# Performance work log

Measured on AMD Instinct MI355X. Metric: run time of the kernel, lower is better.

## Reference

```python
import jax, jax.numpy as jnp
import numpy as np

WS = 8        # window size
NUM_HEADS = 4 # attention heads


def setup_inputs() -> dict:
    key = jax.random.key(0)
    k1, k2, k3 = jax.random.split(key, 3)
    B, N, C = 32, 4096, 128
    x = jax.random.normal(k1, (B, N, C), dtype=jnp.float32)
    w_qkv = jax.random.normal(k2, (3 * C, C), dtype=jnp.float32) * (C ** -0.5)
    w_proj = jax.random.normal(k3, (C, C), dtype=jnp.float32) * (C ** -0.5)
    b_proj = jnp.zeros((C,), dtype=jnp.float32)
    return {"x": x, "w_qkv": w_qkv, "w_proj": w_proj, "b_proj": b_proj, "H": 64, "W": 64}


def reference(x, w_qkv, w_proj, b_proj, H, W):
    B, N, C = x.shape
    ws, nh = WS, NUM_HEADS
    hd = C // nh
    scale = hd ** -0.5
    hg, wg = H // ws, W // ws
    G = hg * wg          # total windows
    S = ws * ws          # tokens per window
    # partition into windows: [B, hg, ws, wg, ws, C] -> [B, G, S, C]
    xg = x.reshape(B, hg, ws, wg, ws, C).transpose(0, 1, 3, 2, 4, 5).reshape(B, G, S, C)
    # qkv projection (no bias)
    qkv = jnp.einsum('bgsc,oc->bgso', xg, w_qkv)
    qkv = qkv.reshape(B, G, S, 3, nh, hd).transpose(3, 0, 1, 4, 2, 5)  # [3,B,G,nh,S,hd]
    q, k, v = qkv[0], qkv[1], qkv[2]
    attn = jnp.einsum('bgnsd,bgntd->bgnst', q, k) * scale
    attn = jax.nn.softmax(attn, axis=-1)
    out = jnp.einsum('bgnst,bgntd->bgnsd', attn, v)
    # [B,G,nh,S,hd] -> [B,G,S,C] -> un-window -> [B,N,C]
    out = out.transpose(0, 1, 3, 2, 4).reshape(B, hg, wg, ws, ws, C)
    out = out.transpose(0, 1, 3, 2, 4, 5).reshape(B, N, C)
    return jnp.einsum('bnc,oc->bno', out, w_proj) + b_proj
```

## Files before the change

### kernel.cpp

```cpp
#include <hip/hip_runtime.h>
#include <cstdint>

typedef short short8 __attribute__((ext_vector_type(8)));
typedef float floatx4 __attribute__((ext_vector_type(4)));
typedef unsigned short ushortx4 __attribute__((ext_vector_type(4)));

__device__ __forceinline__ unsigned short f2bf(float f) {
  union { float f; unsigned u; } v; v.f = f;
  unsigned r = v.u + 0x7FFFu + ((v.u >> 16) & 1u);
  return (unsigned short)(r >> 16);
}
__device__ __forceinline__ float bf2f(unsigned short h) {
  union { unsigned u; float f; } v; v.u = ((unsigned)h) << 16; return v.f;
}

#define MFMA16B(A, B, C) __builtin_amdgcn_mfma_f32_16x16x32_bf16((A), (B), (C), 0, 0, 0)

__global__ void __launch_bounds__(256) prep_weights(const float* __restrict__ wq,
                                                    const float* __restrict__ wp,
                                                    unsigned short* __restrict__ wq_h,
                                                    unsigned short* __restrict__ wp_h) {
  int i = blockIdx.x * 256 + threadIdx.x;
  if (i < 384 * 128) wq_h[i] = f2bf(wq[i]);
  if (i < 128 * 128) wp_h[i] = f2bf(wp[i]);
}

__global__ void __launch_bounds__(256, 2) win_attn(const float* __restrict__ x,
                                                   const unsigned short* __restrict__ wqh,
                                                   const unsigned short* __restrict__ wph,
                                                   const float* __restrict__ bias,
                                                   float* __restrict__ out) {
  __shared__ unsigned short Xh[64][136];
  __shared__ unsigned short Xl[64][136];
  __shared__ unsigned short Qs[64][40];
  __shared__ unsigned short Ks[64][40];
  __shared__ unsigned short Vt[32][72];
  __shared__ unsigned short Ps[64][72];
  __shared__ unsigned short Os[64][136];

  const int tid = threadIdx.x;
  const int bid = blockIdx.x;
  const int b = bid >> 6;
  const int g = bid & 63;
  const int gh = g >> 3, gw = g & 7;
  const size_t base = (size_t)b * 4096 * 128;

  {
    const int r = tid >> 2;
    const int c0 = (tid & 3) * 32;
    const int n = gh * 512 + (r >> 3) * 64 + gw * 8 + (r & 7);
    const float4* xp = (const float4*)(x + base + (size_t)n * 128 + c0);
#pragma unroll
    for (int i = 0; i < 8; ++i) {
      float4 v = xp[i];
      ushortx4 hv, lv;
      hv[0] = f2bf(v.x); lv[0] = f2bf(v.x - bf2f(hv[0]));
      hv[1] = f2bf(v.y); lv[1] = f2bf(v.y - bf2f(hv[1]));
      hv[2] = f2bf(v.z); lv[2] = f2bf(v.z - bf2f(hv[2]));
      hv[3] = f2bf(v.w); lv[3] = f2bf(v.w - bf2f(hv[3]));
      *(ushortx4*)&Xh[r][c0 + i * 4] = hv;
      *(ushortx4*)&Xl[r][c0 + i * 4] = lv;
    }
  }
  __syncthreads();

  const int wv = tid >> 6;
  const int lane = tid & 63;
  const int lr = lane & 15;
  const int lg = lane >> 4;

  short8 ah[4], al[4];
#pragma unroll
  for (int ks = 0; ks < 4; ++ks) {
    ah[ks] = *(const short8*)&Xh[16 * wv + lr][ks * 32 + lg * 8];
    al[ks] = *(const short8*)&Xl[16 * wv + lr][ks * 32 + lg * 8];
  }

  const float scale = 0.17677669529663687f;

#pragma unroll 1
  for (int h = 0; h < 4; ++h) {
#pragma unroll
    for (int m = 0; m < 3; ++m) {
#pragma unroll
      for (int j = 0; j < 2; ++j) {
        floatx4 acc = {0.f, 0.f, 0.f, 0.f};
        const unsigned short* wb =
            wqh + (size_t)(m * 128 + h * 32 + j * 16 + lr) * 128 + lg * 8;
#pragma unroll
        for (int ks = 0; ks < 4; ++ks) {
          short8 bw = *(const short8*)(wb + ks * 32);
          acc = MFMA16B(ah[ks], bw, acc);
          acc = MFMA16B(al[ks], bw, acc);
        }
#pragma unroll
        for (int r = 0; r < 4; ++r) {
          const int s = 16 * wv + 4 * lg + r;
          const int d = j * 16 + lr;
          const unsigned short hv = f2bf(acc[r]);
          if (m == 0)      Qs[s][d] = hv;
          else if (m == 1) Ks[s][d] = hv;
          else             Vt[d][s] = hv;
        }
      }
    }
    __syncthreads();

    floatx4 sc[4];
    {
      short8 bq = *(const short8*)&Qs[16 * wv + lr][lg * 8];
#pragma unroll
      for (int tt = 0; tt < 4; ++tt) {
        short8 ak = *(const short8*)&Ks[16 * tt + lr][lg * 8];
        floatx4 z = {0.f, 0.f, 0.f, 0.f};
        sc[tt] = MFMA16B(ak, bq, z);
      }
    }
    float mx = -1e30f;
#pragma unroll
    for (int tt = 0; tt < 4; ++tt)
#pragma unroll
      for (int r = 0; r < 4; ++r) mx = fmaxf(mx, sc[tt][r]);
    mx = fmaxf(mx, __shfl_xor(mx, 16));
    mx = fmaxf(mx, __shfl_xor(mx, 32));
    float p[4][4];
    float sum = 0.f;
#pragma unroll
    for (int tt = 0; tt < 4; ++tt)
#pragma unroll
      for (int r = 0; r < 4; ++r) {
        float e = __expf(scale * (sc[tt][r] - mx));
        p[tt][r] = e;
        sum += e;
      }
    sum += __shfl_xor(sum, 16);
    sum += __shfl_xor(sum, 32);
    const float inv = 1.f / sum;
#pragma unroll
    for (int tt = 0; tt < 4; ++tt) {
      ushortx4 pv;
#pragma unroll
      for (int r = 0; r < 4; ++r) pv[r] = f2bf(p[tt][r] * inv);
      *(ushortx4*)&Ps[16 * wv + lr][16 * tt + 4 * lg] = pv;
    }
    __syncthreads();

    floatx4 o0 = {0.f, 0.f, 0.f, 0.f}, o1 = {0.f, 0.f, 0.f, 0.f};
#pragma unroll
    for (int ks = 0; ks < 2; ++ks) {
      short8 bp  = *(const short8*)&Ps[16 * wv + lr][ks * 32 + lg * 8];
      short8 av0 = *(const short8*)&Vt[lr][ks * 32 + lg * 8];
      short8 av1 = *(const short8*)&Vt[16 + lr][ks * 32 + lg * 8];
      o0 = MFMA16B(av0, bp, o0);
      o1 = MFMA16B(av1, bp, o1);
    }
#pragma unroll
    for (int r = 0; r < 4; ++r) {
      const int s = 16 * wv + lr;
      Os[s][h * 32 + 4 * lg + r]      = f2bf(o0[r]);
      Os[s][h * 32 + 16 + 4 * lg + r] = f2bf(o1[r]);
    }
    __syncthreads();
  }

  short8 ao[4];
#pragma unroll
  for (int ks = 0; ks < 4; ++ks)
    ao[ks] = *(const short8*)&Os[16 * wv + lr][ks * 32 + lg * 8];
#pragma unroll
  for (int nt = 0; nt < 8; ++nt) {
    floatx4 acc = {0.f, 0.f, 0.f, 0.f};
    const unsigned short* wb = wph + (size_t)(nt * 16 + lr) * 128 + lg * 8;
#pragma unroll
    for (int ks = 0; ks < 4; ++ks)
      acc = MFMA16B(ao[ks], *(const short8*)(wb + ks * 32), acc);
    const float bb = bias[nt * 16 + lr];
#pragma unroll
    for (int r = 0; r < 4; ++r) {
      const int s = 16 * wv + 4 * lg + r;
      const int n = gh * 512 + (s >> 3) * 64 + gw * 8 + (s & 7);
      out[base + (size_t)n * 128 + nt * 16 + lr] = acc[r] + bb;
    }
  }
}

extern "C" void kernel_launch(void* const* d_in, const int* in_sizes, int n_in,
                              void* d_out, int out_size, void* d_ws, size_t ws_size,
                              hipStream_t stream) {
  (void)in_sizes; (void)n_in; (void)out_size; (void)ws_size;
  const float* x  = (const float*)d_in[0];
  const float* wq = (const float*)d_in[1];
  const float* wp = (const float*)d_in[2];
  const float* bp = (const float*)d_in[3];
  float* out = (float*)d_out;
  unsigned short* wq_h = (unsigned short*)d_ws;
  unsigned short* wp_h = wq_h + 384 * 128;
  prep_weights<<<192, 256, 0, stream>>>(wq, wp, wq_h, wp_h);
  win_attn<<<2048, 256, 0, stream>>>(x, wq_h, wp_h, bp, out);
}
```

Measured before the change: 242.1 us.

## Assign one attention head per wavefront and drop per-head block barriers

Work is now split by head instead of by token row. Each wavefront loads and splits the whole 64-token window of x from global memory into hi/lo bf16 fragments itself, computes Q/K/V for its own head, and runs softmax and P·V in private swizzled LDS regions with only compiler fences. This removes the four block-wide barriers per head and the shared X staging buffer, and it pre-scales Q. LDS is packed into one 48KB buffer and launch bounds are raised to 3 blocks per CU. In exchange, every wave reads all of x for the window (4x the global load traffic per block) and the per-wave fragment arrays raise register pressure.

```diff
diff --git a/kernel.cpp b/kernel.cpp
--- a/kernel.cpp
+++ b/kernel.cpp
@@ -15,6 +15,7 @@
 }
 
 #define MFMA16B(A, B, C) __builtin_amdgcn_mfma_f32_16x16x32_bf16((A), (B), (C), 0, 0, 0)
+#define LDS_FENCE() asm volatile("" ::: "memory")
 
 __global__ void __launch_bounds__(256) prep_weights(const float* __restrict__ wq,
                                                     const float* __restrict__ wp,
@@ -25,148 +26,187 @@
   if (i < 128 * 128) wp_h[i] = f2bf(wp[i]);
 }
 
-__global__ void __launch_bounds__(256, 2) win_attn(const float* __restrict__ x,
+__global__ void __launch_bounds__(256, 3) win_attn(const float* __restrict__ x,
                                                    const unsigned short* __restrict__ wqh,
                                                    const unsigned short* __restrict__ wph,
                                                    const float* __restrict__ bias,
                                                    float* __restrict__ out) {
-  __shared__ unsigned short Xh[64][136];
-  __shared__ unsigned short Xl[64][136];
-  __shared__ unsigned short Qs[64][40];
-  __shared__ unsigned short Ks[64][40];
-  __shared__ unsigned short Vt[32][72];
-  __shared__ unsigned short Ps[64][72];
-  __shared__ unsigned short Os[64][136];
+  __shared__ char smem[49152];
 
   const int tid = threadIdx.x;
+  const int wv = tid >> 6;
+  const int lane = tid & 63;
+  const int lr = lane & 15;
+  const int lg = lane >> 4;
+  const int swz = (lr & 7) << 4;
+
   const int bid = blockIdx.x;
   const int b = bid >> 6;
   const int g = bid & 63;
   const int gh = g >> 3, gw = g & 7;
-  const size_t base = (size_t)b * 4096 * 128;
-
-  {
-    const int r = tid >> 2;
-    const int c0 = (tid & 3) * 32;
-    const int n = gh * 512 + (r >> 3) * 64 + gw * 8 + (r & 7);
-    const float4* xp = (const float4*)(x + base + (size_t)n * 128 + c0);
-#pragma unroll
-    for (int i = 0; i < 8; ++i) {
-      float4 v = xp[i];
-      ushortx4 hv, lv;
-      hv[0] = f2bf(v.x); lv[0] = f2bf(v.x - bf2f(hv[0]));
-      hv[1] = f2bf(v.y); lv[1] = f2bf(v.y - bf2f(hv[1]));
-      hv[2] = f2bf(v.z); lv[2] = f2bf(v.z - bf2f(hv[2]));
-      hv[3] = f2bf(v.w); lv[3] = f2bf(v.w - bf2f(hv[3]));
-      *(ushortx4*)&Xh[r][c0 + i * 4] = hv;
-      *(ushortx4*)&Xl[r][c0 + i * 4] = lv;
-    }
-  }
-  __syncthreads();
-
-  const int wv = tid >> 6;
-  const int lane = tid & 63;
-  const int lr = lane & 15;
-  const int lg = lane >> 4;
-
-  short8 ah[4], al[4];
-#pragma unroll
-  for (int ks = 0; ks < 4; ++ks) {
-    ah[ks] = *(const short8*)&Xh[16 * wv + lr][ks * 32 + lg * 8];
-    al[ks] = *(const short8*)&Xl[16 * wv + lr][ks * 32 + lg * 8];
-  }
-
-  const float scale = 0.17677669529663687f;
-
-#pragma unroll 1
-  for (int h = 0; h < 4; ++h) {
+  const size_t base = (size_t)b * (4096 * 128);
+
+  char* regA = smem + wv * 8192;
+  char* regV = smem + 32768 + wv * 4096;
+  char* osb  = smem;
+
+  const float SCALE = 0.17677669529663687f;
+
+#pragma unroll
+  for (int mt = 0; mt < 4; ++mt) {
+    const int s = mt * 16 + lr;
+    const int n = gh * 512 + (s >> 3) * 64 + gw * 8 + (s & 7);
+    const float* xp = x + base + (size_t)n * 128 + lg * 8;
+    short8 ah[4], al[4];
+#pragma unroll
+    for (int ks = 0; ks < 4; ++ks) {
+      float4 u = *(const float4*)(xp + ks * 32);
+      float4 w = *(const float4*)(xp + ks * 32 + 4);
+      float f[8] = {u.x, u.y, u.z, u.w, w.x, w.y, w.z, w.w};
+      short8 hh, ll;
+#pragma unroll
+      for (int j = 0; j < 8; ++j) {
+        unsigned short hb = f2bf(f[j]);
+        hh[j] = (short)hb;
+        ll[j] = (short)f2bf(f[j] - bf2f(hb));
+      }
+      ah[ks] = hh;
+      al[ks] = ll;
+    }
 #pragma unroll
     for (int m = 0; m < 3; ++m) {
 #pragma unroll
-      for (int j = 0; j < 2; ++j) {
+      for (int jt = 0; jt < 2; ++jt) {
         floatx4 acc = {0.f, 0.f, 0.f, 0.f};
         const unsigned short* wb =
-            wqh + (size_t)(m * 128 + h * 32 + j * 16 + lr) * 128 + lg * 8;
+            wqh + (size_t)(m * 128 + wv * 32 + jt * 16 + lr) * 128 + lg * 8;
 #pragma unroll
         for (int ks = 0; ks < 4; ++ks) {
           short8 bw = *(const short8*)(wb + ks * 32);
           acc = MFMA16B(ah[ks], bw, acc);
           acc = MFMA16B(al[ks], bw, acc);
         }
-#pragma unroll
-        for (int r = 0; r < 4; ++r) {
-          const int s = 16 * wv + 4 * lg + r;
-          const int d = j * 16 + lr;
-          const unsigned short hv = f2bf(acc[r]);
-          if (m == 0)      Qs[s][d] = hv;
-          else if (m == 1) Ks[s][d] = hv;
-          else             Vt[d][s] = hv;
+        if (m == 2) {
+          ushortx4 vv;
+#pragma unroll
+          for (int r = 0; r < 4; ++r) vv[r] = f2bf(acc[r]);
+          const int d = jt * 16 + lr;
+          *(ushortx4*)(regV + ((d * 128 + mt * 32 + lg * 8) ^ swz)) = vv;
+        } else {
+#pragma unroll
+          for (int r = 0; r < 4; ++r) {
+            const int s0 = mt * 16 + 4 * lg + r;
+            const int col = (m ? 32 : 0) + jt * 16 + lr;
+            const float v = (m == 0) ? acc[r] * SCALE : acc[r];
+            *(unsigned short*)(regA + ((s0 * 128 + col * 2) ^ ((s0 & 7) << 4))) =
+                f2bf(v);
+          }
         }
       }
     }
-    __syncthreads();
-
-    floatx4 sc[4];
-    {
-      short8 bq = *(const short8*)&Qs[16 * wv + lr][lg * 8];
-#pragma unroll
-      for (int tt = 0; tt < 4; ++tt) {
-        short8 ak = *(const short8*)&Ks[16 * tt + lr][lg * 8];
-        floatx4 z = {0.f, 0.f, 0.f, 0.f};
-        sc[tt] = MFMA16B(ak, bq, z);
+  }
+
+  LDS_FENCE();
+
+  short8 kf[4], qf[4];
+#pragma unroll
+  for (int i = 0; i < 4; ++i) {
+    const int row = i * 16 + lr;
+    qf[i] = *(const short8*)(regA + ((row * 128 + 16 * lg) ^ swz));
+    kf[i] = *(const short8*)(regA + ((row * 128 + 64 + 16 * lg) ^ swz));
+  }
+  floatx4 sc[4][4];
+#pragma unroll
+  for (int mt = 0; mt < 4; ++mt)
+#pragma unroll
+    for (int nt = 0; nt < 4; ++nt) {
+      floatx4 z = {0.f, 0.f, 0.f, 0.f};
+      sc[mt][nt] = MFMA16B(kf[mt], qf[nt], z);
+    }
+
+  float mx[4], inv[4];
+#pragma unroll
+  for (int nt = 0; nt < 4; ++nt) {
+    float m0 = -1e30f;
+#pragma unroll
+    for (int mt = 0; mt < 4; ++mt)
+#pragma unroll
+      for (int r = 0; r < 4; ++r) m0 = fmaxf(m0, sc[mt][nt][r]);
+    m0 = fmaxf(m0, __shfl_xor(m0, 16));
+    m0 = fmaxf(m0, __shfl_xor(m0, 32));
+    mx[nt] = m0;
+  }
+#pragma unroll
+  for (int nt = 0; nt < 4; ++nt) {
+    float s0 = 0.f;
+#pragma unroll
+    for (int mt = 0; mt < 4; ++mt)
+#pragma unroll
+      for (int r = 0; r < 4; ++r) {
+        float e = __expf(sc[mt][nt][r] - mx[nt]);
+        sc[mt][nt][r] = e;
+        s0 += e;
       }
-    }
-    float mx = -1e30f;
-#pragma unroll
-    for (int tt = 0; tt < 4; ++tt)
-#pragma unroll
-      for (int r = 0; r < 4; ++r) mx = fmaxf(mx, sc[tt][r]);
-    mx = fmaxf(mx, __shfl_xor(mx, 16));
-    mx = fmaxf(mx, __shfl_xor(mx, 32));
-    float p[4][4];
-    float sum = 0.f;
-#pragma unroll
-    for (int tt = 0; tt < 4; ++tt)
-#pragma unroll
-      for (int r = 0; r < 4; ++r) {
-        float e = __expf(scale * (sc[tt][r] - mx));
-        p[tt][r] = e;
-        sum += e;
-      }
-    sum += __shfl_xor(sum, 16);
-    sum += __shfl_xor(sum, 32);
-    const float inv = 1.f / sum;
-#pragma unroll
-    for (int tt = 0; tt < 4; ++tt) {
+    s0 += __shfl_xor(s0, 16);
+    s0 += __shfl_xor(s0, 32);
+    inv[nt] = 1.f / s0;
+  }
+
+#pragma unroll
+  for (int nt = 0; nt < 4; ++nt) {
+    const int row = nt * 16 + lr;
+#pragma unroll
+    for (int mt = 0; mt < 4; ++mt) {
       ushortx4 pv;
 #pragma unroll
-      for (int r = 0; r < 4; ++r) pv[r] = f2bf(p[tt][r] * inv);
-      *(ushortx4*)&Ps[16 * wv + lr][16 * tt + 4 * lg] = pv;
-    }
-    __syncthreads();
-
-    floatx4 o0 = {0.f, 0.f, 0.f, 0.f}, o1 = {0.f, 0.f, 0.f, 0.f};
-#pragma unroll
-    for (int ks = 0; ks < 2; ++ks) {
-      short8 bp  = *(const short8*)&Ps[16 * wv + lr][ks * 32 + lg * 8];
-      short8 av0 = *(const short8*)&Vt[lr][ks * 32 + lg * 8];
-      short8 av1 = *(const short8*)&Vt[16 + lr][ks * 32 + lg * 8];
-      o0 = MFMA16B(av0, bp, o0);
-      o1 = MFMA16B(av1, bp, o1);
-    }
-#pragma unroll
-    for (int r = 0; r < 4; ++r) {
-      const int s = 16 * wv + lr;
-      Os[s][h * 32 + 4 * lg + r]      = f2bf(o0[r]);
-      Os[s][h * 32 + 16 + 4 * lg + r] = f2bf(o1[r]);
-    }
-    __syncthreads();
-  }
+      for (int r = 0; r < 4; ++r) pv[r] = f2bf(sc[mt][nt][r] * inv[nt]);
+      *(ushortx4*)(regA + ((row * 128 + mt * 32 + lg * 8) ^ swz)) = pv;
+    }
+  }
+
+  LDS_FENCE();
+
+  short8 vf[2][2], pf[4][2];
+#pragma unroll
+  for (int dt = 0; dt < 2; ++dt)
+#pragma unroll
+    for (int ks = 0; ks < 2; ++ks)
+      vf[dt][ks] = *(const short8*)(regV + (((16 * dt + lr) * 128 + ks * 64 + 16 * lg) ^ swz));
+#pragma unroll
+  for (int st = 0; st < 4; ++st)
+#pragma unroll
+    for (int ks = 0; ks < 2; ++ks)
+      pf[st][ks] = *(const short8*)(regA + (((16 * st + lr) * 128 + ks * 64 + 16 * lg) ^ swz));
+  floatx4 ot[2][4];
+#pragma unroll
+  for (int dt = 0; dt < 2; ++dt)
+#pragma unroll
+    for (int st = 0; st < 4; ++st) {
+      floatx4 z = {0.f, 0.f, 0.f, 0.f};
+      ot[dt][st] = z;
+#pragma unroll
+      for (int ks = 0; ks < 2; ++ks)
+        ot[dt][st] = MFMA16B(vf[dt][ks], pf[st][ks], ot[dt][st]);
+    }
+
+  __syncthreads();
+
+#pragma unroll
+  for (int st = 0; st < 4; ++st)
+#pragma unroll
+    for (int dt = 0; dt < 2; ++dt) {
+      ushortx4 ov;
+#pragma unroll
+      for (int r = 0; r < 4; ++r) ov[r] = f2bf(ot[dt][st][r]);
+      *(ushortx4*)(osb + (16 * st + lr) * 272 + (wv * 32 + dt * 16 + 4 * lg) * 2) = ov;
+    }
+
+  __syncthreads();
 
   short8 ao[4];
 #pragma unroll
   for (int ks = 0; ks < 4; ++ks)
-    ao[ks] = *(const short8*)&Os[16 * wv + lr][ks * 32 + lg * 8];
+    ao[ks] = *(const short8*)(osb + (16 * wv + lr) * 272 + ks * 64 + 16 * lg);
 #pragma unroll
   for (int nt = 0; nt < 8; ++nt) {
     floatx4 acc = {0.f, 0.f, 0.f, 0.f};
@@ -177,8 +217,8 @@
     const float bb = bias[nt * 16 + lr];
 #pragma unroll
     for (int r = 0; r < 4; ++r) {
-      const int s = 16 * wv + 4 * lg + r;
-      const int n = gh * 512 + (s >> 3) * 64 + gw * 8 + (s & 7);
+      const int s0 = 16 * wv + 4 * lg + r;
+      const int n = gh * 512 + (s0 >> 3) * 64 + gw * 8 + (s0 & 7);
       out[base + (size_t)n * 128 + nt * 16 + lr] = acc[r] + bb;
     }
   }
```

After: 249.1 us. +2.9%, slower.
